# Kernel optimization log

Measured on AMD Instinct MI355X. Metric: run time of the kernel, lower is better.

## Reference

```python
import jax, jax.numpy as jnp
import numpy as np

N_NODES = 100000

def gcn_conv(h, row, col, w, W, b, n):
    # linear transform then symmetric-normalized weighted aggregation (PyG GCNConv)
    h = h @ W                                   # [N, F_out]
    deg = jax.ops.segment_sum(w, row, num_segments=n)          # weighted in-degree [N]
    dinv = jnp.where(deg > 0, jax.lax.rsqrt(deg), 0.0)
    norm = dinv[row] * w * dinv[col]            # [E]
    msg = norm[:, None] * h[col]                # gather+scale, [E, F_out]
    return jax.ops.segment_sum(msg, row, num_segments=n) + b

def setup_inputs() -> dict:
    key = jax.random.key(0)
    ks = jax.random.split(key, 6)
    N, E, D, H = N_NODES, 1600000, 128, 128
    x = jax.random.normal(ks[0], (N, D), dtype=jnp.float32)
    edge_index = jax.random.randint(ks[1], (2, E), 0, N, dtype=jnp.int64)
    edge_weight = jax.random.uniform(ks[2], (E,), dtype=jnp.float32)
    W1 = jax.random.normal(ks[3], (D, H), dtype=jnp.float32) / np.sqrt(D)
    b1 = jnp.zeros((H,), dtype=jnp.float32)
    W2 = jax.random.normal(ks[4], (H, H), dtype=jnp.float32) / np.sqrt(H)
    b2 = jnp.zeros((H,), dtype=jnp.float32)
    return {"x": x, "edge_index": edge_index, "edge_weight": edge_weight,
            "W1": W1, "b1": b1, "W2": W2, "b2": b2}

def reference(x, edge_index, edge_weight, W1, b1, W2, b2):
    n = x.shape[0]
    # add self-loops with weight 1 (PyG gcn_norm default)
    loops = jnp.arange(n, dtype=edge_index.dtype)
    row = jnp.concatenate([edge_index[0], loops])
    col = jnp.concatenate([edge_index[1], loops])
    w = jnp.concatenate([edge_weight, jnp.ones((n,), dtype=edge_weight.dtype)])
    h = gcn_conv(x, row, col, w, W1, b1, n)
    h = jax.nn.relu(h)  # dropout is identity in eval mode
    h = gcn_conv(h, row, col, w, W2, b2, n)
    return h
```

## Files before the change

### kernel.cpp

```cpp
#include <hip/hip_runtime.h>


constexpr int N_NODES = 100000;
constexpr int FD = 128;
constexpr int NPAD = 100352;
constexpr int CAP = 48;
constexpr int PSH = 7;
constexpr int PROWS = 128;
constexpr int NP = (N_NODES + PROWS - 1) / PROWS;
constexpr int RCAP = 2560;
constexpr int PSTRIDE = 16;
constexpr int EPB = 4096;
constexpr int EPT = 16;

typedef __attribute__((ext_vector_type(8))) short bf16x8;
typedef __attribute__((ext_vector_type(4))) float f32x4;
#define MFMA16(a, b, c) __builtin_amdgcn_mfma_f32_16x16x32_bf16(a, b, c, 0, 0, 0)

static __device__ __forceinline__ unsigned f2bf(float x) {
  unsigned u = __float_as_uint(x);
  return (u + 0x7FFFu + ((u >> 16) & 1u)) >> 16;
}
static __device__ __forceinline__ float bflo(unsigned u) {
  return __uint_as_float(u << 16);
}
static __device__ __forceinline__ float bfhi(unsigned u) {
  return __uint_as_float(u & 0xFFFF0000u);
}

__global__ __launch_bounds__(256) void k_part(const int* __restrict__ row,
                                              const int* __restrict__ col,
                                              const float* __restrict__ w,
                                              int* __restrict__ pcnt,
                                              int2* __restrict__ rec, int E) {
  __shared__ int lcnt[NP];
  const int t = threadIdx.x;
  const int e0 = blockIdx.x * EPB;
  for (int p = t; p < NP; p += 256) lcnt[p] = 0;
  __syncthreads();

  int packed[EPT];
  int cols[EPT];
  int ws[EPT];
#pragma unroll
  for (int i = 0; i < EPT; i++) {
    int e = e0 + i * 256 + t;
    packed[i] = -1;
    if (e < E) {
      int r = row[e];
      cols[i] = col[e];
      ws[i] = __float_as_int(w[e]);
      int part = r >> PSH, rl = r & (PROWS - 1);
      int off = atomicAdd(&lcnt[part], 1);
      packed[i] = part | (rl << 10) | (off << 17);
    }
  }
  __syncthreads();

  for (int p = t; p < NP; p += 256) {
    int c = lcnt[p];
    int base = 0;
    if (c) base = atomicAdd(&pcnt[p * PSTRIDE], c);
    lcnt[p] = base;
  }
  __syncthreads();

#pragma unroll
  for (int i = 0; i < EPT; i++) {
    int pk = packed[i];
    if (pk >= 0) {
      int part = pk & 0x3FF;
      int rl = (pk >> 10) & 0x7F;
      int pos = lcnt[part] + (pk >> 17);
      if (pos < RCAP)
        rec[(size_t)part * RCAP + pos] = make_int2(cols[i] | (rl << 20), ws[i]);
    }
  }
}

__global__ __launch_bounds__(256) void k_bin(const int* __restrict__ pcnt,
                                             const int2* __restrict__ rec,
                                             int2* __restrict__ bucket,
                                             int* __restrict__ cnt,
                                             float* __restrict__ dinv) {
  __shared__ int lcnt[PROWS];
  __shared__ float lsum[PROWS];
  const int part = blockIdx.x, t = threadIdx.x;
  if (t < PROWS) { lcnt[t] = 0; lsum[t] = 0.f; }
  __syncthreads();
  const int n = min(pcnt[part * PSTRIDE], RCAP);
  const int row0 = part << PSH;
  const int2* rp = rec + (size_t)part * RCAP;
  for (int j = t; j < n; j += 256) {
    int2 R = rp[j];
    int rl = R.x >> 20;
    int c = R.x & 0xFFFFF;
    int p = atomicAdd(&lcnt[rl], 1);
    if (p < CAP) bucket[(size_t)(row0 + rl) * CAP + p] = make_int2(c, R.y);
    atomicAdd(&lsum[rl], __int_as_float(R.y));
  }
  __syncthreads();
  int i = row0 + t;
  if (t < PROWS && i < N_NODES) {
    cnt[i] = min(lcnt[t], CAP);
    dinv[i] = rsqrtf(lsum[t] + 1.0f);
  }
}

__global__ __launch_bounds__(128) void k_prep(const float* __restrict__ W1,
                                              const float* __restrict__ W2,
                                              ushort* __restrict__ W1hT,
                                              ushort* __restrict__ W1lT,
                                              ushort* __restrict__ W2hT,
                                              ushort* __restrict__ W2lT,
                                              int* __restrict__ pcnt) {
  int b = blockIdx.x;
  int k = threadIdx.x;
  int zid = b * 128 + k;
  if (zid < 16384) pcnt[zid] = 0;
  int n0 = b & (FD - 1);
  const float* W = (b < FD) ? W1 : W2;
  ushort* Wh = (b < FD) ? W1hT : W2hT;
  ushort* Wl = (b < FD) ? W1lT : W2lT;
  float v = W[k * FD + n0];
  unsigned h = f2bf(v);
  float r = v - bflo(h);
  Wh[n0 * FD + k] = (ushort)h;
  Wl[n0 * FD + k] = (ushort)f2bf(r);
}

__global__ __launch_bounds__(512) void k_gemm(const float* __restrict__ X,
                                              const ushort* __restrict__ WhT,
                                              const ushort* __restrict__ WlT,
                                              const float* __restrict__ dinv,
                                              ushort* __restrict__ Yb,
                                              int relu_in) {
  __shared__ ushort sl[32768];
  ushort* lwh = sl;
  ushort* lwl = sl + 16384;
  const int t = threadIdx.x;
  const int wid = t >> 6;
  const int lane = t & 63;
  const int g = lane >> 4;
  const int lr = lane & 15;

  {
    const uint4* gh = (const uint4*)WhT;
    const uint4* gl = (const uint4*)WlT;
#pragma unroll
    for (int i = 0; i < 4; i++) {
      int idx = i * 512 + t;
      int byte = idx * 16;
      int n = byte >> 8;
      int swz = byte ^ (((n >> 3) & 7) << 4);
      *(uint4*)((char*)lwh + swz) = gh[idx];
      *(uint4*)((char*)lwl + swz) = gl[idx];
    }
  }
  __syncthreads();

#pragma unroll
  for (int tile = 0; tile < 2; tile++) {
    const size_t rb = (size_t)blockIdx.x * 256 + tile * 128;
    const size_t row_base = rb + wid * 16 + lr;
    const size_t rowc = row_base < N_NODES ? row_base : 0;
    const float* xr = X + rowc * FD;
    float xv[4][8];
#pragma unroll
    for (int ks = 0; ks < 4; ks++) {
      *(float4*)&xv[ks][0] = *(const float4*)(xr + ks * 32 + g * 8);
      *(float4*)&xv[ks][4] = *(const float4*)(xr + ks * 32 + g * 8 + 4);
    }

    f32x4 acc[8];
#pragma unroll
    for (int nf = 0; nf < 8; nf++) acc[nf] = (f32x4)(0.f);

#pragma unroll
    for (int ks = 0; ks < 4; ks++) {
      bf16x8 a_h, a_l;
#pragma unroll
      for (int j = 0; j < 8; j++) {
        float v = xv[ks][j];
        if (relu_in) v = fmaxf(v, 0.f);
        unsigned hb_ = f2bf(v);
        float r = v - bflo(hb_);
        a_h[j] = (short)hb_;
        a_l[j] = (short)f2bf(r);
      }
#pragma unroll
      for (int nf = 0; nf < 8; nf++) {
        int n = lr * 8 + nf;
        int byte = n * 256 + ks * 64 + g * 16;
        int swz = byte ^ (((n >> 3) & 7) << 4);
        bf16x8 bh = *(const bf16x8*)((const char*)lwh + swz);
        bf16x8 bl = *(const bf16x8*)((const char*)lwl + swz);
        acc[nf] = MFMA16(a_h, bh, acc[nf]);
        acc[nf] = MFMA16(a_l, bh, acc[nf]);
        acc[nf] = MFMA16(a_h, bl, acc[nf]);
      }
    }

    const size_t rw = rb + wid * 16;
#pragma unroll
    for (int r = 0; r < 4; r++) {
      size_t rg = rw + g * 4 + r;
      if (rg < N_NODES) {
        float dv = dinv[rg];
        uint4 o;
        o.x = f2bf(acc[0][r] * dv) | (f2bf(acc[1][r] * dv) << 16);
        o.y = f2bf(acc[2][r] * dv) | (f2bf(acc[3][r] * dv) << 16);
        o.z = f2bf(acc[4][r] * dv) | (f2bf(acc[5][r] * dv) << 16);
        o.w = f2bf(acc[6][r] * dv) | (f2bf(acc[7][r] * dv) << 16);
        *(uint4*)(Yb + rg * FD + lr * 8) = o;
      }
    }
  }
}

static __device__ __forceinline__ void acc8(float* a, float s, uint4 g) {
  a[0] += s * bflo(g.x);
  a[1] += s * bfhi(g.x);
  a[2] += s * bflo(g.y);
  a[3] += s * bfhi(g.y);
  a[4] += s * bflo(g.z);
  a[5] += s * bfhi(g.z);
  a[6] += s * bflo(g.w);
  a[7] += s * bfhi(g.w);
}

__global__ __launch_bounds__(256, 4) void k_gather(
    const ushort* __restrict__ hb, const int* __restrict__ cnt,
    const int2* __restrict__ bucket, const float* __restrict__ dinv,
    const float* __restrict__ b, float* __restrict__ out) {
  int t = blockIdx.x * 256 + threadIdx.x;
  int i = t >> 4, q = t & 15;
  if (i >= N_NODES) return;
  float di = dinv[i];
  const uint4* H = (const uint4*)hb;
  uint4 hv = H[(size_t)i * 16 + q];
  float a[8];
  a[0] = bflo(hv.x); a[1] = bfhi(hv.x);
  a[2] = bflo(hv.y); a[3] = bfhi(hv.y);
  a[4] = bflo(hv.z); a[5] = bfhi(hv.z);
  a[6] = bflo(hv.w); a[7] = bfhi(hv.w);
  const int c = min(cnt[i], CAP);
  const int2* bk = bucket + (size_t)i * CAP;
  const int nb = (c + 7) >> 3;

  int2 cur[8];
  if (nb > 0) {
#pragma unroll
    for (int j = 0; j < 4; j++)
      *(int4*)&cur[j * 2] = *(const int4*)&bk[j * 2];
  }
  for (int bt = 0; bt < nb; bt++) {
    int2 nxt[8];
    if (bt + 1 < nb) {
#pragma unroll
      for (int j = 0; j < 4; j++)
        *(int4*)&nxt[j * 2] = *(const int4*)&bk[(bt + 1) * 8 + j * 2];
    }
    const int base = bt * 8;
    int idx[8];
    float wv[8];
#pragma unroll
    for (int j = 0; j < 8; j++) {
      bool v = (base + j) < c;
      idx[j] = v ? cur[j].x : i;
      wv[j] = v ? __int_as_float(cur[j].y) : 0.f;
    }
    uint4 g[8];
#pragma unroll
    for (int j = 0; j < 8; j++) g[j] = H[(size_t)idx[j] * 16 + q];
#pragma unroll
    for (int j = 0; j < 8; j++) acc8(a, wv[j], g[j]);
#pragma unroll
    for (int j = 0; j < 8; j++) cur[j] = nxt[j];
  }
  float4 b0 = ((const float4*)b)[q * 2];
  float4 b1 = ((const float4*)b)[q * 2 + 1];
  float* o = out + (size_t)i * FD + q * 8;
  float4 o0, o1;
  o0.x = di * a[0] + b0.x; o0.y = di * a[1] + b0.y;
  o0.z = di * a[2] + b0.z; o0.w = di * a[3] + b0.w;
  o1.x = di * a[4] + b1.x; o1.y = di * a[5] + b1.y;
  o1.z = di * a[6] + b1.z; o1.w = di * a[7] + b1.w;
  ((float4*)o)[0] = o0;
  ((float4*)o)[1] = o1;
}

extern "C" void kernel_launch(void* const* d_in, const int* in_sizes, int n_in,
                              void* d_out, int out_size, void* d_ws, size_t ws_size,
                              hipStream_t stream) {
  const float* x  = (const float*)d_in[0];
  const int*   ei = (const int*)d_in[1];
  const float* ew = (const float*)d_in[2];
  const float* W1 = (const float*)d_in[3];
  const float* b1 = (const float*)d_in[4];
  const float* W2 = (const float*)d_in[5];
  const float* b2 = (const float*)d_in[6];
  float* out = (float*)d_out;

  const int E = in_sizes[2];
  const int* row = ei;
  const int* col = ei + E;

  int*    pcnt   = (int*)d_ws;
  float*  dinv   = (float*)(pcnt + 16384);
  int*    cnt    = (int*)(dinv + NPAD);
  int2*   bucket = (int2*)(cnt + NPAD);
  int2*   rec    = bucket + (size_t)NPAD * CAP;
  ushort* hb     = (ushort*)(rec + (size_t)NP * RCAP);
  ushort* w1ht   = hb + (size_t)NPAD * FD;
  ushort* w1lt   = w1ht + FD * FD;
  ushort* w2ht   = w1lt + FD * FD;
  ushort* w2lt   = w2ht + FD * FD;

  k_prep<<<2 * FD, FD, 0, stream>>>(W1, W2, w1ht, w1lt, w2ht, w2lt, pcnt);
  const int part_grid = (E + EPB - 1) / EPB;
  k_part<<<part_grid, 256, 0, stream>>>(row, col, ew, pcnt, rec, E);
  k_bin<<<NP, 256, 0, stream>>>(pcnt, rec, bucket, cnt, dinv);

  const int gemm_grid = (N_NODES + 255) / 256;
  const int ga_grid   = (N_NODES * 16 + 255) / 256;

  k_gemm<<<gemm_grid, 512, 0, stream>>>(x, w1ht, w1lt, dinv, hb, 0);
  k_gather<<<ga_grid, 256, 0, stream>>>(hb, cnt, bucket, dinv, b1, out);
  k_gemm<<<gemm_grid, 512, 0, stream>>>(out, w2ht, w2lt, dinv, hb, 1);
  k_gather<<<ga_grid, 256, 0, stream>>>(hb, cnt, bucket, dinv, b2, out);
}
```

Baseline: 322.8 us.

## Merge weight prep into partition and binning into first GEMM kernel

Weight bf16 split/transposition now runs as extra blocks of the partition kernel, and degree binning runs as extra blocks alongside the first GEMM. To remove the GEMM's dependency on dinv, the source-side normalization moves into the gather, which does an extra dinv lookup per edge, and the destination scale is applied at the start. pcnt zeroing becomes a memset. This cuts two kernel launches and lets independent work overlap, at the cost of extra random dinv loads in the gather.

```diff
diff --git a/kernel.cpp b/kernel.cpp
--- a/kernel.cpp
+++ b/kernel.cpp
@@ -28,13 +28,31 @@
   return __uint_as_float(u & 0xFFFF0000u);
 }
 
-__global__ __launch_bounds__(256) void k_part(const int* __restrict__ row,
-                                              const int* __restrict__ col,
-                                              const float* __restrict__ w,
-                                              int* __restrict__ pcnt,
-                                              int2* __restrict__ rec, int E) {
+__global__ __launch_bounds__(256) void k_part(
+    const int* __restrict__ row, const int* __restrict__ col,
+    const float* __restrict__ w, int* __restrict__ pcnt,
+    int2* __restrict__ rec, int E,
+    const float* __restrict__ W1, const float* __restrict__ W2,
+    ushort* __restrict__ W1hT, ushort* __restrict__ W1lT,
+    ushort* __restrict__ W2hT, ushort* __restrict__ W2lT) {
+  const int pgrid = (E + EPB - 1) / EPB;
+  const int t = threadIdx.x;
+  if ((int)blockIdx.x >= pgrid) {
+    int b2 = blockIdx.x - pgrid;
+    int col2 = b2 * 2 + (t >> 7);
+    int k = t & 127;
+    int n0 = col2 & (FD - 1);
+    const float* W = (col2 < FD) ? W1 : W2;
+    ushort* Wh = (col2 < FD) ? W1hT : W2hT;
+    ushort* Wl = (col2 < FD) ? W1lT : W2lT;
+    float v = W[k * FD + n0];
+    unsigned h = f2bf(v);
+    float r = v - bflo(h);
+    Wh[n0 * FD + k] = (ushort)h;
+    Wl[n0 * FD + k] = (ushort)f2bf(r);
+    return;
+  }
   __shared__ int lcnt[NP];
-  const int t = threadIdx.x;
   const int e0 = blockIdx.x * EPB;
   for (int p = t; p < NP; p += 256) lcnt[p] = 0;
   __syncthreads();
@@ -78,64 +96,10 @@
   }
 }
 
-__global__ __launch_bounds__(256) void k_bin(const int* __restrict__ pcnt,
-                                             const int2* __restrict__ rec,
-                                             int2* __restrict__ bucket,
-                                             int* __restrict__ cnt,
-                                             float* __restrict__ dinv) {
-  __shared__ int lcnt[PROWS];
-  __shared__ float lsum[PROWS];
-  const int part = blockIdx.x, t = threadIdx.x;
-  if (t < PROWS) { lcnt[t] = 0; lsum[t] = 0.f; }
-  __syncthreads();
-  const int n = min(pcnt[part * PSTRIDE], RCAP);
-  const int row0 = part << PSH;
-  const int2* rp = rec + (size_t)part * RCAP;
-  for (int j = t; j < n; j += 256) {
-    int2 R = rp[j];
-    int rl = R.x >> 20;
-    int c = R.x & 0xFFFFF;
-    int p = atomicAdd(&lcnt[rl], 1);
-    if (p < CAP) bucket[(size_t)(row0 + rl) * CAP + p] = make_int2(c, R.y);
-    atomicAdd(&lsum[rl], __int_as_float(R.y));
-  }
-  __syncthreads();
-  int i = row0 + t;
-  if (t < PROWS && i < N_NODES) {
-    cnt[i] = min(lcnt[t], CAP);
-    dinv[i] = rsqrtf(lsum[t] + 1.0f);
-  }
-}
-
-__global__ __launch_bounds__(128) void k_prep(const float* __restrict__ W1,
-                                              const float* __restrict__ W2,
-                                              ushort* __restrict__ W1hT,
-                                              ushort* __restrict__ W1lT,
-                                              ushort* __restrict__ W2hT,
-                                              ushort* __restrict__ W2lT,
-                                              int* __restrict__ pcnt) {
-  int b = blockIdx.x;
-  int k = threadIdx.x;
-  int zid = b * 128 + k;
-  if (zid < 16384) pcnt[zid] = 0;
-  int n0 = b & (FD - 1);
-  const float* W = (b < FD) ? W1 : W2;
-  ushort* Wh = (b < FD) ? W1hT : W2hT;
-  ushort* Wl = (b < FD) ? W1lT : W2lT;
-  float v = W[k * FD + n0];
-  unsigned h = f2bf(v);
-  float r = v - bflo(h);
-  Wh[n0 * FD + k] = (ushort)h;
-  Wl[n0 * FD + k] = (ushort)f2bf(r);
-}
-
-__global__ __launch_bounds__(512) void k_gemm(const float* __restrict__ X,
-                                              const ushort* __restrict__ WhT,
-                                              const ushort* __restrict__ WlT,
-                                              const float* __restrict__ dinv,
-                                              ushort* __restrict__ Yb,
-                                              int relu_in) {
-  __shared__ ushort sl[32768];
+static __device__ __forceinline__ void gemm_body(
+    const float* __restrict__ X, const ushort* __restrict__ WhT,
+    const ushort* __restrict__ WlT, ushort* __restrict__ Yb,
+    int relu_in, int bid, ushort* sl) {
   ushort* lwh = sl;
   ushort* lwl = sl + 16384;
   const int t = threadIdx.x;
@@ -161,7 +125,7 @@
 
 #pragma unroll
   for (int tile = 0; tile < 2; tile++) {
-    const size_t rb = (size_t)blockIdx.x * 256 + tile * 128;
+    const size_t rb = (size_t)bid * 256 + tile * 128;
     const size_t row_base = rb + wid * 16 + lr;
     const size_t rowc = row_base < N_NODES ? row_base : 0;
     const float* xr = X + rowc * FD;
@@ -206,15 +170,58 @@
     for (int r = 0; r < 4; r++) {
       size_t rg = rw + g * 4 + r;
       if (rg < N_NODES) {
-        float dv = dinv[rg];
         uint4 o;
-        o.x = f2bf(acc[0][r] * dv) | (f2bf(acc[1][r] * dv) << 16);
-        o.y = f2bf(acc[2][r] * dv) | (f2bf(acc[3][r] * dv) << 16);
-        o.z = f2bf(acc[4][r] * dv) | (f2bf(acc[5][r] * dv) << 16);
-        o.w = f2bf(acc[6][r] * dv) | (f2bf(acc[7][r] * dv) << 16);
+        o.x = f2bf(acc[0][r]) | (f2bf(acc[1][r]) << 16);
+        o.y = f2bf(acc[2][r]) | (f2bf(acc[3][r]) << 16);
+        o.z = f2bf(acc[4][r]) | (f2bf(acc[5][r]) << 16);
+        o.w = f2bf(acc[6][r]) | (f2bf(acc[7][r]) << 16);
         *(uint4*)(Yb + rg * FD + lr * 8) = o;
       }
     }
+  }
+}
+
+__global__ __launch_bounds__(512) void k_gemm(const float* __restrict__ X,
+                                              const ushort* __restrict__ WhT,
+                                              const ushort* __restrict__ WlT,
+                                              ushort* __restrict__ Yb,
+                                              int relu_in) {
+  __shared__ ushort sl[32768];
+  gemm_body(X, WhT, WlT, Yb, relu_in, blockIdx.x, sl);
+}
+
+__global__ __launch_bounds__(512) void k_bingemm(
+    const float* __restrict__ X, const ushort* __restrict__ WhT,
+    const ushort* __restrict__ WlT, ushort* __restrict__ Yb,
+    const int* __restrict__ pcnt, const int2* __restrict__ rec,
+    int2* __restrict__ bucket, int* __restrict__ cnt,
+    float* __restrict__ dinv, int ggrid) {
+  __shared__ ushort sl[32768];
+  if ((int)blockIdx.x < ggrid) {
+    gemm_body(X, WhT, WlT, Yb, 0, blockIdx.x, sl);
+    return;
+  }
+  int* lcnt = (int*)sl;
+  float* lsum = (float*)(sl + 256);
+  const int part = blockIdx.x - ggrid, t = threadIdx.x;
+  if (t < PROWS) { lcnt[t] = 0; lsum[t] = 0.f; }
+  __syncthreads();
+  const int n = min(pcnt[part * PSTRIDE], RCAP);
+  const int row0 = part << PSH;
+  const int2* rp = rec + (size_t)part * RCAP;
+  for (int j = t; j < n; j += 512) {
+    int2 R = rp[j];
+    int rl = R.x >> 20;
+    int c = R.x & 0xFFFFF;
+    int p = atomicAdd(&lcnt[rl], 1);
+    if (p < CAP) bucket[(size_t)(row0 + rl) * CAP + p] = make_int2(c, R.y);
+    atomicAdd(&lsum[rl], __int_as_float(R.y));
+  }
+  __syncthreads();
+  int i = row0 + t;
+  if (t < PROWS && i < N_NODES) {
+    cnt[i] = min(lcnt[t], CAP);
+    dinv[i] = rsqrtf(lsum[t] + 1.0f);
   }
 }
 
@@ -240,10 +247,10 @@
   const uint4* H = (const uint4*)hb;
   uint4 hv = H[(size_t)i * 16 + q];
   float a[8];
-  a[0] = bflo(hv.x); a[1] = bfhi(hv.x);
-  a[2] = bflo(hv.y); a[3] = bfhi(hv.y);
-  a[4] = bflo(hv.z); a[5] = bfhi(hv.z);
-  a[6] = bflo(hv.w); a[7] = bfhi(hv.w);
+  a[0] = di * bflo(hv.x); a[1] = di * bfhi(hv.x);
+  a[2] = di * bflo(hv.y); a[3] = di * bfhi(hv.y);
+  a[4] = di * bflo(hv.z); a[5] = di * bfhi(hv.z);
+  a[6] = di * bflo(hv.w); a[7] = di * bfhi(hv.w);
   const int c = min(cnt[i], CAP);
   const int2* bk = bucket + (size_t)i * CAP;
   const int nb = (c + 7) >> 3;
@@ -273,8 +280,11 @@
     uint4 g[8];
 #pragma unroll
     for (int j = 0; j < 8; j++) g[j] = H[(size_t)idx[j] * 16 + q];
-#pragma unroll
-    for (int j = 0; j < 8; j++) acc8(a, wv[j], g[j]);
+    float s[8];
+#pragma unroll
+    for (int j = 0; j < 8; j++) s[j] = wv[j] * dinv[idx[j]];
+#pragma unroll
+    for (int j = 0; j < 8; j++) acc8(a, s[j], g[j]);
 #pragma unroll
     for (int j = 0; j < 8; j++) cur[j] = nxt[j];
   }
@@ -317,16 +327,16 @@
   ushort* w2ht   = w1lt + FD * FD;
   ushort* w2lt   = w2ht + FD * FD;
 
-  k_prep<<<2 * FD, FD, 0, stream>>>(W1, W2, w1ht, w1lt, w2ht, w2lt, pcnt);
+  hipMemsetAsync(pcnt, 0, 16384 * sizeof(int), stream);
   const int part_grid = (E + EPB - 1) / EPB;
-  k_part<<<part_grid, 256, 0, stream>>>(row, col, ew, pcnt, rec, E);
-  k_bin<<<NP, 256, 0, stream>>>(pcnt, rec, bucket, cnt, dinv);
-
   const int gemm_grid = (N_NODES + 255) / 256;
   const int ga_grid   = (N_NODES * 16 + 255) / 256;
 
-  k_gemm<<<gemm_grid, 512, 0, stream>>>(x, w1ht, w1lt, dinv, hb, 0);
+  k_part<<<part_grid + 128, 256, 0, stream>>>(row, col, ew, pcnt, rec, E,
+                                              W1, W2, w1ht, w1lt, w2ht, w2lt);
+  k_bingemm<<<gemm_grid + NP, 512, 0, stream>>>(x, w1ht, w1lt, hb, pcnt, rec,
+                                                bucket, cnt, dinv, gemm_grid);
   k_gather<<<ga_grid, 256, 0, stream>>>(hb, cnt, bucket, dinv, b1, out);
-  k_gemm<<<gemm_grid, 512, 0, stream>>>(out, w2ht, w2lt, dinv, hb, 1);
+  k_gemm<<<gemm_grid, 512, 0, stream>>>(out, w2ht, w2lt, hb, 1);
   k_gather<<<ga_grid, 256, 0, stream>>>(hb, cnt, bucket, dinv, b2, out);
 }
```

New measurement: 360.2 us. +11.6%, slower.
